# Kernel tuning notes

Measured on AMD Instinct MI355X. Metric: run time of the kernel, lower is better.

## Reference

```python
import jax, jax.numpy as jnp
import numpy as np
from jax import lax

# LIF neuron parameters (norse LIFParameters defaults)
DT = 0.001
TAU_SYN_INV = 200.0
TAU_MEM_INV = 100.0
V_LEAK = 0.0
V_TH = 1.0
V_RESET = 0.0
ALPHA = 100.0  # SuperSpike surrogate slope


@jax.custom_vjp
def spike(x):
    # heaviside step with SuperSpike surrogate gradient
    return (x > 0).astype(x.dtype)

def _spike_fwd(x):
    return (x > 0).astype(x.dtype), x

def _spike_bwd(x, g):
    sg = 1.0 / (ALPHA * jnp.abs(x) + 1.0) ** 2
    return (g * sg,)

spike.defvjp(_spike_fwd, _spike_bwd)


def setup_inputs() -> dict:
    key = jax.random.key(0)
    T, B, N = 1024, 32, 2048
    input_tensor = jax.random.normal(key, (T, B, N), dtype=jnp.float32)
    return {"input_tensor": input_tensor}


def reference(input_tensor):
    # state_fallback: zero (v, i) shaped like one timestep
    v0 = jnp.zeros_like(input_tensor[0])
    i0 = jnp.zeros_like(input_tensor[0])

    def step(carry, x_t):
        v, i = carry
        # membrane integration: dv = dt * tau_mem_inv * ((v_leak - v) + i)
        v_dec = v + DT * TAU_MEM_INV * ((V_LEAK - v) + i)
        # synaptic current decay: di = -dt * tau_syn_inv * i
        i_dec = i * (1.0 - DT * TAU_SYN_INV)
        # spike + reset
        z = spike(v_dec - V_TH)
        v_new = (1.0 - z) * v_dec + z * V_RESET
        # inject input current
        i_new = i_dec + x_t
        return (v_new, i_new), z

    (v_f, i_f), spikes = lax.scan(step, (v0, i0), input_tensor)
    # matches SNN.forward: (stacked outputs, final state)
    return spikes, v_f, i_f
```

## Files before the change

kernel.cpp:

```cpp
#include <hip/hip_runtime.h>


#define TT 1024
#define BN 65536
#define BN2 (BN / 2)
#define U  16

__global__ __launch_bounds__(128, 1) void snn_lif_kernel(
    const float* __restrict__ xf,
    float* __restrict__ outf)
{
    const int idx = blockIdx.x * 128 + threadIdx.x;
    const float2* __restrict__ xp = (const float2*)xf + idx;
    float2* __restrict__ sp = (float2*)outf + idx;

    float v0 = 0.0f, v1 = 0.0f;
    float i0 = 0.0f, i1 = 0.0f;

    const float c_mem = 0.1f;
    const float c_syn = 0.8f;

    auto step = [&](float& v, float& i, float xin) -> float {
        float dv    = __fmul_rn(c_mem, __fadd_rn(__fsub_rn(0.0f, v), i));
        float v_dec = __fadd_rn(v, dv);
        float i_dec = __fmul_rn(i, c_syn);
        bool fired  = (v_dec > 1.0f);
        v = fired ? 0.0f : v_dec;
        i = __fadd_rn(i_dec, xin);
        return fired ? 1.0f : 0.0f;
    };

    float2 xa[U], xb[U];

    #pragma unroll
    for (int k = 0; k < U; ++k)
        xa[k] = xp[(size_t)k * BN2];

    #pragma unroll 1
    for (int t0 = 0; t0 < TT; t0 += 2 * U) {
        #pragma unroll
        for (int k = 0; k < U; ++k)
            xb[k] = xp[(size_t)(t0 + U + k) * BN2];

        #pragma unroll
        for (int k = 0; k < U; ++k) {
            float2 z;
            z.x = step(v0, i0, xa[k].x);
            z.y = step(v1, i1, xa[k].y);
            sp[(size_t)(t0 + k) * BN2] = z;
        }

        if (t0 + 2 * U < TT) {
            #pragma unroll
            for (int k = 0; k < U; ++k)
                xa[k] = xp[(size_t)(t0 + 2 * U + k) * BN2];
        }

        #pragma unroll
        for (int k = 0; k < U; ++k) {
            float2 z;
            z.x = step(v0, i0, xb[k].x);
            z.y = step(v1, i1, xb[k].y);
            sp[(size_t)(t0 + U + k) * BN2] = z;
        }
    }

    float2* vf = (float2*)(outf + (size_t)TT * BN) + idx;
    float2* iff = (float2*)(outf + (size_t)TT * BN + BN) + idx;
    *vf = make_float2(v0, v1);
    *iff = make_float2(i0, i1);
}

extern "C" void kernel_launch(void* const* d_in, const int* in_sizes, int n_in,
                              void* d_out, int out_size, void* d_ws, size_t ws_size,
                              hipStream_t stream) {
    const float* x = (const float*)d_in[0];
    float* out = (float*)d_out;
    snn_lif_kernel<<<BN2 / 128, 128, 0, stream>>>(x, out);
}
```

Baseline: 423.6 us.

## Use one neuron per thread with scalar nontemporal loads and stores

Switches from two neurons per thread with float2 accesses to one neuron per thread with scalar float accesses, launching 256 blocks of 256 threads instead of 256 blocks of 128. This doubles the thread count so more wavefronts are available to hide memory latency on the streaming time loop. It also marks input loads and spike stores as nontemporal to avoid polluting caches. The trade-off is narrower per-thread memory transactions and more instructions per byte moved.

New measurement: 414.6 us. 2.1% less time.

```diff
diff --git a/kernel.cpp b/kernel.cpp
--- a/kernel.cpp
+++ b/kernel.cpp
@@ -3,24 +3,22 @@
 
 #define TT 1024
 #define BN 65536
-#define BN2 (BN / 2)
 #define U  16
 
-__global__ __launch_bounds__(128, 1) void snn_lif_kernel(
+__global__ __launch_bounds__(256, 1) void snn_lif_kernel(
     const float* __restrict__ xf,
     float* __restrict__ outf)
 {
-    const int idx = blockIdx.x * 128 + threadIdx.x;
-    const float2* __restrict__ xp = (const float2*)xf + idx;
-    float2* __restrict__ sp = (float2*)outf + idx;
+    const int idx = blockIdx.x * 256 + threadIdx.x;
+    const float* __restrict__ xp = xf + idx;
+    float* __restrict__ sp = outf + idx;
 
-    float v0 = 0.0f, v1 = 0.0f;
-    float i0 = 0.0f, i1 = 0.0f;
+    float v = 0.0f, i = 0.0f;
 
     const float c_mem = 0.1f;
     const float c_syn = 0.8f;
 
-    auto step = [&](float& v, float& i, float xin) -> float {
+    auto step = [&](float xin) -> float {
         float dv    = __fmul_rn(c_mem, __fadd_rn(__fsub_rn(0.0f, v), i));
         float v_dec = __fadd_rn(v, dv);
         float i_dec = __fmul_rn(i, c_syn);
@@ -30,45 +28,40 @@
         return fired ? 1.0f : 0.0f;
     };
 
-    float2 xa[U], xb[U];
+    float xa[U], xb[U];
 
     #pragma unroll
     for (int k = 0; k < U; ++k)
-        xa[k] = xp[(size_t)k * BN2];
+        xa[k] = __builtin_nontemporal_load(&xp[(size_t)k * BN]);
 
     #pragma unroll 1
     for (int t0 = 0; t0 < TT; t0 += 2 * U) {
         #pragma unroll
         for (int k = 0; k < U; ++k)
-            xb[k] = xp[(size_t)(t0 + U + k) * BN2];
+            xb[k] = __builtin_nontemporal_load(&xp[(size_t)(t0 + U + k) * BN]);
 
         #pragma unroll
         for (int k = 0; k < U; ++k) {
-            float2 z;
-            z.x = step(v0, i0, xa[k].x);
-            z.y = step(v1, i1, xa[k].y);
-            sp[(size_t)(t0 + k) * BN2] = z;
+            float z = step(xa[k]);
+            __builtin_nontemporal_store(z, &sp[(size_t)(t0 + k) * BN]);
         }
 
         if (t0 + 2 * U < TT) {
             #pragma unroll
             for (int k = 0; k < U; ++k)
-                xa[k] = xp[(size_t)(t0 + 2 * U + k) * BN2];
+                xa[k] = __builtin_nontemporal_load(
+                    &xp[(size_t)(t0 + 2 * U + k) * BN]);
         }
 
         #pragma unroll
         for (int k = 0; k < U; ++k) {
-            float2 z;
-            z.x = step(v0, i0, xb[k].x);
-            z.y = step(v1, i1, xb[k].y);
-            sp[(size_t)(t0 + U + k) * BN2] = z;
+            float z = step(xb[k]);
+            __builtin_nontemporal_store(z, &sp[(size_t)(t0 + U + k) * BN]);
         }
     }
 
-    float2* vf = (float2*)(outf + (size_t)TT * BN) + idx;
-    float2* iff = (float2*)(outf + (size_t)TT * BN + BN) + idx;
-    *vf = make_float2(v0, v1);
-    *iff = make_float2(i0, i1);
+    outf[(size_t)TT * BN + idx] = v;
+    outf[(size_t)TT * BN + BN + idx] = i;
 }
 
 extern "C" void kernel_launch(void* const* d_in, const int* in_sizes, int n_in,
@@ -76,5 +69,5 @@
                               hipStream_t stream) {
     const float* x = (const float*)d_in[0];
     float* out = (float*)d_out;
-    snn_lif_kernel<<<BN2 / 128, 128, 0, stream>>>(x, out);
+    snn_lif_kernel<<<BN / 256, 256, 0, stream>>>(x, out);
 }
```
